# Kernel tuning notes

Hardware: AMD Instinct MI355X
Metric: run time of the kernel (lower is better)

The kernel has to match this reference:

```python
import jax, jax.numpy as jnp
import numpy as np

L, H, C, HS, V, BS = 4, 8, 512, 64, 32000, 2048  # layers, heads, n_embd, head_size, vocab, block_size
B, T = 2, 2048


def _ln(x, g, b, eps=1e-5):
    m = jnp.mean(x, axis=-1, keepdims=True)
    v = jnp.var(x, axis=-1, keepdims=True)
    return (x - m) * jax.lax.rsqrt(v + eps) * g + b


def setup_inputs() -> dict:
    key = jax.random.key(0)
    ks = jax.random.split(key, 12)
    s = 0.02
    f = jnp.float32
    return {
        "idx": jax.random.randint(ks[0], (B, T), 0, V),
        "tok_emb": jax.random.normal(ks[1], (V, C), f) * s,
        "pos_emb": jax.random.normal(ks[2], (BS, C), f) * s,
        "ln1_g": jnp.ones((L, C), f), "ln1_b": jnp.zeros((L, C), f),
        "wq": jax.random.normal(ks[3], (L, H, C, HS), f) * s,
        "wk": jax.random.normal(ks[4], (L, H, C, HS), f) * s,
        "wv": jax.random.normal(ks[5], (L, H, C, HS), f) * s,
        "proj_w": jax.random.normal(ks[6], (L, C, C), f) * s,
        "proj_b": jnp.zeros((L, C), f),
        "ln2_g": jnp.ones((L, C), f), "ln2_b": jnp.zeros((L, C), f),
        "ff_w1": jax.random.normal(ks[7], (L, C, 4 * C), f) * s,
        "ff_b1": jnp.zeros((L, 4 * C), f),
        "ff_w2": jax.random.normal(ks[8], (L, 4 * C, C), f) * s,
        "ff_b2": jnp.zeros((L, C), f),
        "ffln_g": jnp.ones((L, C), f), "ffln_b": jnp.zeros((L, C), f),
        "lm_w": jax.random.normal(ks[9], (C, V), f) * s,
        "lm_b": jnp.zeros((V,), f),
    }


def reference(idx, tok_emb, pos_emb, ln1_g, ln1_b, wq, wk, wv, proj_w, proj_b,
              ln2_g, ln2_b, ff_w1, ff_b1, ff_w2, ff_b2, ffln_g, ffln_b, lm_w, lm_b):
    Tn = idx.shape[1]
    x = tok_emb[idx] + pos_emb[:Tn]  # [B,T,C]
    causal = jnp.tril(jnp.ones((Tn, Tn), bool))
    for l in range(L):
        h = _ln(x, ln1_g[l], ln1_b[l])
        q = jnp.einsum('btc,hcd->bhtd', h, wq[l])
        k = jnp.einsum('btc,hcd->bhtd', h, wk[l])
        v = jnp.einsum('btc,hcd->bhtd', h, wv[l])
        # NOTE: original module does NOT scale by 1/sqrt(head_size)
        wei = jnp.einsum('bhtd,bhsd->bhts', q, k)
        wei = jnp.where(causal, wei, -jnp.inf)
        wei = jax.nn.softmax(wei, axis=-1)
        att = jnp.einsum('bhts,bhsd->bhtd', wei, v)  # [B,H,T,HS]
        att = att.transpose(0, 2, 1, 3).reshape(x.shape[0], Tn, C)
        x = x + att @ proj_w[l].T + proj_b[l]
        h2 = _ln(x, ln2_g[l], ln2_b[l])
        ff = jax.nn.relu(h2 @ ff_w1[l] + ff_b1[l]) @ ff_w2[l] + ff_b2[l]
        ff = _ln(ff, ffln_g[l], ffln_b[l])  # FeedForward has trailing LayerNorm
        x = x + ff
    logits = x @ lm_w + lm_b  # [B,T,V]
    return logits
```

## Files before the change

### kernel.cpp

```cpp
#include <hip/hip_runtime.h>
#include <math.h>

#define NLAYER 4
#define NH     8
#define CDIM   512
#define HS     64
#define VOCAB  32000
#define BB     2
#define TT     2048
#define MROWS  (BB*TT)
#define QKVW   (3*CDIM)

typedef __attribute__((ext_vector_type(8))) short bf16x8;
typedef __attribute__((ext_vector_type(4))) float f32x4;

__device__ __forceinline__ unsigned short f2bf(float f) {
    unsigned int u = __float_as_uint(f);
    u += 0x7FFF + ((u >> 16) & 1);
    return (unsigned short)(u >> 16);
}

#define GLOAD16(g, l) __builtin_amdgcn_global_load_lds( \
    (const __attribute__((address_space(1))) void*)(g), \
    (__attribute__((address_space(3))) void*)(l), 16, 0, 0)

template<int FLAGS, bool OUTBF>
__global__ __launch_bounds__(256) void mfma_gemm(
    const unsigned short* __restrict__ A, int lda,
    const unsigned short* __restrict__ Bt, int ldb,
    const float* __restrict__ bias,
    void* __restrict__ Cout, int ldc,
    const float* __restrict__ resid,
    int K)
{
    __shared__ unsigned short As[128*64];
    __shared__ unsigned short Bs[128*64];
    const int tid = threadIdx.x;
    const int w = tid >> 6, l = tid & 63;
    const int wr = w >> 1, wc = w & 1;
    const long m0 = (long)blockIdx.y * 128;
    const long n0 = (long)blockIdx.x * 128;
    const int srow = l >> 3;
    const int scol = (l & 7) << 3;
    const unsigned short* Ab = A + m0*lda;
    const unsigned short* Bb = Bt + n0*ldb;
    const int fr = l & 15;
    const int fk = (l >> 4) << 3;

    f32x4 acc[4][4];
    #pragma unroll
    for (int m = 0; m < 4; m++)
        #pragma unroll
        for (int n = 0; n < 4; n++) acc[m][n] = (f32x4)0.0f;

    for (int k0 = 0; k0 < K; k0 += 64) {
        __syncthreads();
        #pragma unroll
        for (int i = 0; i < 4; i++) {
            int seg = w*4 + i;
            GLOAD16(Ab + (long)(seg*8 + srow)*lda + k0 + scol, As + seg*512);
            GLOAD16(Bb + (long)(seg*8 + srow)*ldb + k0 + scol, Bs + seg*512);
        }
        __syncthreads();
        #pragma unroll
        for (int kk = 0; kk < 2; kk++) {
            bf16x8 af[4], bf[4];
            #pragma unroll
            for (int m = 0; m < 4; m++)
                af[m] = *(const bf16x8*)&As[(wr*64 + m*16 + fr)*64 + kk*32 + fk];
            #pragma unroll
            for (int n = 0; n < 4; n++)
                bf[n] = *(const bf16x8*)&Bs[(wc*64 + n*16 + fr)*64 + kk*32 + fk];
            #pragma unroll
            for (int m = 0; m < 4; m++)
                #pragma unroll
                for (int n = 0; n < 4; n++)
                    acc[m][n] = __builtin_amdgcn_mfma_f32_16x16x32_bf16(
                        af[m], bf[n], acc[m][n], 0, 0, 0);
        }
    }

    const int rg = (l >> 4) << 2;
    #pragma unroll
    for (int n = 0; n < 4; n++) {
        long gn = n0 + wc*64 + n*16 + fr;
        float bv = (FLAGS & 1) ? bias[gn] : 0.f;
        #pragma unroll
        for (int m = 0; m < 4; m++) {
            #pragma unroll
            for (int r = 0; r < 4; r++) {
                long gm = m0 + wr*64 + m*16 + rg + r;
                float val = acc[m][n][r] + bv;
                if (FLAGS & 2) val = fmaxf(val, 0.f);
                if (FLAGS & 4) val += resid[gm*ldc + gn];
                if (OUTBF) ((unsigned short*)Cout)[gm*ldc + gn] = f2bf(val);
                else       ((float*)Cout)[gm*ldc + gn] = val;
            }
        }
    }
}

__global__ __launch_bounds__(256) void mfma_gemm_qkv(
    const unsigned short* __restrict__ A,
    const unsigned short* __restrict__ Bt,
    unsigned short* __restrict__ qh,
    unsigned short* __restrict__ kh,
    unsigned short* __restrict__ vt)
{
    __shared__ unsigned short As[128*64];
    __shared__ unsigned short Bs[128*64];
    const int tid = threadIdx.x;
    const int w = tid >> 6, l = tid & 63;
    const int wr = w >> 1, wc = w & 1;
    const long m0 = (long)blockIdx.y * 128;
    const long n0 = (long)blockIdx.x * 128;
    const int srow = l >> 3;
    const int scol = (l & 7) << 3;
    const unsigned short* Ab = A + m0*CDIM;
    const unsigned short* Bb = Bt + n0*CDIM;
    const int fr = l & 15;
    const int fk = (l >> 4) << 3;

    f32x4 acc[4][4];
    #pragma unroll
    for (int m = 0; m < 4; m++)
        #pragma unroll
        for (int n = 0; n < 4; n++) acc[m][n] = (f32x4)0.0f;

    for (int k0 = 0; k0 < CDIM; k0 += 64) {
        __syncthreads();
        #pragma unroll
        for (int i = 0; i < 4; i++) {
            int seg = w*4 + i;
            GLOAD16(Ab + (long)(seg*8 + srow)*CDIM + k0 + scol, As + seg*512);
            GLOAD16(Bb + (long)(seg*8 + srow)*CDIM + k0 + scol, Bs + seg*512);
        }
        __syncthreads();
        #pragma unroll
        for (int kk = 0; kk < 2; kk++) {
            bf16x8 af[4], bf[4];
            #pragma unroll
            for (int m = 0; m < 4; m++)
                af[m] = *(const bf16x8*)&As[(wr*64 + m*16 + fr)*64 + kk*32 + fk];
            #pragma unroll
            for (int n = 0; n < 4; n++)
                bf[n] = *(const bf16x8*)&Bs[(wc*64 + n*16 + fr)*64 + kk*32 + fk];
            #pragma unroll
            for (int m = 0; m < 4; m++)
                #pragma unroll
                for (int n = 0; n < 4; n++)
                    acc[m][n] = __builtin_amdgcn_mfma_f32_16x16x32_bf16(
                        af[m], bf[n], acc[m][n], 0, 0, 0);
        }
    }

    const int rg = (l >> 4) << 2;
    #pragma unroll
    for (int n = 0; n < 4; n++) {
        int gn = (int)(n0 + wc*64 + n*16 + fr);
        int which = gn >> 9, hh = (gn >> 6) & 7, d = gn & 63;
        #pragma unroll
        for (int m = 0; m < 4; m++) {
            #pragma unroll
            for (int r = 0; r < 4; r++) {
                int gm = (int)(m0 + wr*64 + m*16 + rg + r);
                int b = gm >> 11, t = gm & (TT-1);
                int head = b*NH + hh;
                unsigned short val = f2bf(acc[m][n][r]);
                if (which == 0)      qh[((long)head*TT + t)*HS + d] = val;
                else if (which == 1) kh[((long)head*TT + t)*HS + d] = val;
                else                 vt[((long)head*HS + d)*TT + t] = val;
            }
        }
    }
}

__global__ __launch_bounds__(256) void attn_mfma(
    const unsigned short* __restrict__ qh,
    const unsigned short* __restrict__ kh,
    const unsigned short* __restrict__ vt,
    unsigned short* __restrict__ att)
{
    __shared__ unsigned short Ks[2][64*64];
    __shared__ unsigned short Vts[2][64*64];
    __shared__ unsigned short Ps[4][32*72];
    const int tid = threadIdx.x;
    const int w = tid >> 6, l = tid & 63;
    const int fr = l & 15, g = l >> 4;
    const int head = blockIdx.y;
    const int b = head >> 3, hh = head & 7;
    const int qt0 = blockIdx.x * 128;
    const int qw = qt0 + w*32;
    const unsigned short* Qb = qh + (long)head*TT*HS;
    const unsigned short* Kb = kh + (long)head*TT*HS;
    const unsigned short* Vb = vt + (long)head*HS*TT;

    bf16x8 aq[2][2];
    #pragma unroll
    for (int mt = 0; mt < 2; mt++)
        #pragma unroll
        for (int ks = 0; ks < 2; ks++)
            aq[mt][ks] = *(const bf16x8*)&Qb[(long)(qw + mt*16 + fr)*HS + ks*32 + g*8];

    f32x4 acc_o[2][4];
    float mrun[2][4], lsum[2][4];
    #pragma unroll
    for (int mt = 0; mt < 2; mt++) {
        #pragma unroll
        for (int r = 0; r < 4; r++) { mrun[mt][r] = -INFINITY; lsum[mt][r] = 0.f; }
        #pragma unroll
        for (int n = 0; n < 4; n++) acc_o[mt][n] = (f32x4)0.0f;
    }

    const int nch = 2*blockIdx.x + 2;
    const int srow = l >> 3;
    const int scol = ((l & 7) ^ (srow & 7)) << 3;

    auto stage = [&](int c, int buf) {
        int s0_ = c*64;
        #pragma unroll
        for (int i = 0; i < 2; i++) {
            int rb = i*32 + w*8;
            GLOAD16(Kb + (long)(s0_ + rb + srow)*HS + scol, &Ks[buf][rb*64]);
            GLOAD16(Vb + (long)(rb + srow)*TT + s0_ + scol, &Vts[buf][rb*64]);
        }
    };

    stage(0, 0);
    for (int c = 0; c < nch; c++) {
        const int s0 = c*64;
        const int buf = c & 1;
        __syncthreads();
        if (c + 1 < nch) stage(c+1, (c+1)&1);
        if (s0 > qw + 31) continue;

        bf16x8 bk[4][2];
        #pragma unroll
        for (int n = 0; n < 4; n++)
            #pragma unroll
            for (int ks = 0; ks < 2; ks++) {
                int row = n*16 + fr;
                int u = (ks*4 + g) ^ (row & 7);
                bk[n][ks] = *(const bf16x8*)&Ks[buf][row*64 + u*8];
            }
        f32x4 sc[2][4];
        #pragma unroll
        for (int mt = 0; mt < 2; mt++)
            #pragma unroll
            for (int n = 0; n < 4; n++) sc[mt][n] = (f32x4)0.0f;
        #pragma unroll
        for (int ks = 0; ks < 2; ks++)
            #pragma unroll
            for (int mt = 0; mt < 2; mt++)
                #pragma unroll
                for (int n = 0; n < 4; n++)
                    sc[mt][n] = __builtin_amdgcn_mfma_f32_16x16x32_bf16(
                        aq[mt][ks], bk[n][ks], sc[mt][n], 0, 0, 0);

        #pragma unroll
        for (int mt = 0; mt < 2; mt++) {
            #pragma unroll
            for (int r = 0; r < 4; r++) {
                int q = qw + mt*16 + g*4 + r;
                float rmax = -INFINITY;
                #pragma unroll
                for (int n = 0; n < 4; n++) {
                    float v = sc[mt][n][r];
                    v = (s0 + n*16 + fr <= q) ? v : -INFINITY;
                    sc[mt][n][r] = v;
                    rmax = fmaxf(rmax, v);
                }
                #pragma unroll
                for (int off = 8; off >= 1; off >>= 1)
                    rmax = fmaxf(rmax, __shfl_xor(rmax, off));
                float mnew = fmaxf(mrun[mt][r], rmax);
                float scale = __expf(mrun[mt][r] - mnew);
                float ps = 0.f;
                #pragma unroll
                for (int n = 0; n < 4; n++) {
                    float p = __expf(sc[mt][n][r] - mnew);
                    sc[mt][n][r] = p;
                    ps += p;
                }
                #pragma unroll
                for (int off = 8; off >= 1; off >>= 1)
                    ps += __shfl_xor(ps, off);
                lsum[mt][r] = lsum[mt][r]*scale + ps;
                mrun[mt][r] = mnew;
                #pragma unroll
                for (int n = 0; n < 4; n++) acc_o[mt][n][r] *= scale;
            }
        }

        #pragma unroll
        for (int mt = 0; mt < 2; mt++)
            #pragma unroll
            for (int n = 0; n < 4; n++)
                #pragma unroll
                for (int r = 0; r < 4; r++)
                    Ps[w][(mt*16 + g*4 + r)*72 + n*16 + fr] = f2bf(sc[mt][n][r]);

        bf16x8 ap[2][2], bv[4][2];
        #pragma unroll
        for (int mt = 0; mt < 2; mt++)
            #pragma unroll
            for (int ks = 0; ks < 2; ks++)
                ap[mt][ks] = *(const bf16x8*)&Ps[w][(mt*16 + fr)*72 + ks*32 + g*8];
        #pragma unroll
        for (int n = 0; n < 4; n++)
            #pragma unroll
            for (int ks = 0; ks < 2; ks++) {
                int row = n*16 + fr;
                int u = (ks*4 + g) ^ (row & 7);
                bv[n][ks] = *(const bf16x8*)&Vts[buf][row*64 + u*8];
            }
        #pragma unroll
        for (int ks = 0; ks < 2; ks++)
            #pragma unroll
            for (int mt = 0; mt < 2; mt++)
                #pragma unroll
                for (int n = 0; n < 4; n++)
                    acc_o[mt][n] = __builtin_amdgcn_mfma_f32_16x16x32_bf16(
                        ap[mt][ks], bv[n][ks], acc_o[mt][n], 0, 0, 0);
    }

    #pragma unroll
    for (int mt = 0; mt < 2; mt++)
        #pragma unroll
        for (int n = 0; n < 4; n++)
            #pragma unroll
            for (int r = 0; r < 4; r++) {
                int t = qw + mt*16 + g*4 + r;
                int d = n*16 + fr;
                att[((long)b*TT + t)*CDIM + hh*HS + d] =
                    f2bf(acc_o[mt][n][r] / lsum[mt][r]);
            }
}

__global__ __launch_bounds__(256) void transpose_cast(
    const float* __restrict__ in, unsigned short* __restrict__ out,
    int R, int Cn, long in_z1, long in_z2, long out_z1, long out_z2, int z2n)
{
    const int z = blockIdx.z;
    const int z1 = z / z2n, z2 = z % z2n;
    const float* ip = in + (long)z1*in_z1 + (long)z2*in_z2;
    unsigned short* op = out + (long)z1*out_z1 + (long)z2*out_z2;
    __shared__ float tile[32][33];
    const int tx = threadIdx.x & 31, ty = threadIdx.x >> 5;
    const long r0 = (long)blockIdx.y*32, c0 = (long)blockIdx.x*32;
    #pragma unroll
    for (int i = 0; i < 4; i++)
        tile[ty + i*8][tx] = ip[(r0 + ty + i*8)*Cn + c0 + tx];
    __syncthreads();
    #pragma unroll
    for (int i = 0; i < 4; i++)
        op[(c0 + ty + i*8)*R + r0 + tx] = f2bf(tile[tx][ty + i*8]);
}

__global__ __launch_bounds__(256) void cast_kernel(
    const float* __restrict__ in, unsigned short* __restrict__ out, long n)
{
    long i = ((long)blockIdx.x*256 + threadIdx.x) * 4;
    if (i >= n) return;
    float4 v = *(const float4*)(in + i);
    ushort4 u = make_ushort4(f2bf(v.x), f2bf(v.y), f2bf(v.z), f2bf(v.w));
    *(ushort4*)(out + i) = u;
}

__global__ void embed_kernel(const int* __restrict__ idx,
                             const float* __restrict__ tok,
                             const float* __restrict__ pos,
                             float* __restrict__ x)
{
    const int r = blockIdx.x;
    const int t = r & (TT-1);
    const long tr = idx[r];
    const float* te = tok + tr*CDIM;
    const float* pe = pos + (long)t*CDIM;
    float* xo = x + (long)r*CDIM;
    for (int c = threadIdx.x; c < CDIM; c += blockDim.x)
        xo[c] = te[c] + pe[c];
}

template<int MODE>
__global__ __launch_bounds__(256) void ln_kernel(
    const float* __restrict__ in, const float* __restrict__ g,
    const float* __restrict__ bb, void* __restrict__ outp)
{
    const int wave = threadIdx.x >> 6;
    const int lane = threadIdx.x & 63;
    const long r = (long)blockIdx.x*4 + wave;
    const float* xr = in + r*CDIM;
    float vals[8];
    float s = 0.f;
    #pragma unroll
    for (int i = 0; i < 8; i++) { vals[i] = xr[lane + i*64]; s += vals[i]; }
    #pragma unroll
    for (int o = 32; o >= 1; o >>= 1) s += __shfl_xor(s, o);
    const float mean = s * (1.f/CDIM);
    float vs = 0.f;
    #pragma unroll
    for (int i = 0; i < 8; i++) { float d = vals[i]-mean; vs += d*d; }
    #pragma unroll
    for (int o = 32; o >= 1; o >>= 1) vs += __shfl_xor(vs, o);
    const float rstd = rsqrtf(vs*(1.f/CDIM) + 1e-5f);
    #pragma unroll
    for (int i = 0; i < 8; i++) {
        int c = lane + i*64;
        float nv = (vals[i]-mean)*rstd*g[c] + bb[c];
        if (MODE == 1) ((unsigned short*)outp)[r*CDIM + c] = f2bf(nv);
        else           ((float*)outp)[r*CDIM + c] += nv;
    }
}

extern "C" void kernel_launch(void* const* d_in, const int* in_sizes, int n_in,
                              void* d_out, int out_size, void* d_ws, size_t ws_size,
                              hipStream_t stream)
{
    const int*   idx   = (const int*)  d_in[0];
    const float* tok   = (const float*)d_in[1];
    const float* pos   = (const float*)d_in[2];
    const float* ln1g  = (const float*)d_in[3];
    const float* ln1b  = (const float*)d_in[4];
    const float* wq    = (const float*)d_in[5];
    const float* wk    = (const float*)d_in[6];
    const float* wv    = (const float*)d_in[7];
    const float* projw = (const float*)d_in[8];
    const float* projb = (const float*)d_in[9];
    const float* ln2g  = (const float*)d_in[10];
    const float* ln2b  = (const float*)d_in[11];
    const float* ffw1  = (const float*)d_in[12];
    const float* ffb1  = (const float*)d_in[13];
    const float* ffw2  = (const float*)d_in[14];
    const float* ffb2  = (const float*)d_in[15];
    const float* flng  = (const float*)d_in[16];
    const float* flnb  = (const float*)d_in[17];
    const float* lmw   = (const float*)d_in[18];
    const float* lmb   = (const float*)d_in[19];
    float* out = (float*)d_out;

    char* wp = (char*)d_ws;
    float* x  = (float*)wp;           wp += (size_t)MROWS*CDIM*4;
    float* ff = (float*)wp;           wp += (size_t)MROWS*CDIM*4;
    unsigned short* h     = (unsigned short*)wp; wp += (size_t)MROWS*CDIM*2;
    unsigned short* lmt   = (unsigned short*)wp; wp += (size_t)VOCAB*CDIM*2;
    unsigned short* ff1t  = (unsigned short*)wp; wp += (size_t)NLAYER*4*CDIM*CDIM*2;
    unsigned short* ff2t  = (unsigned short*)wp; wp += (size_t)NLAYER*4*CDIM*CDIM*2;
    unsigned short* qkvt  = (unsigned short*)wp; wp += (size_t)NLAYER*QKVW*CDIM*2;
    unsigned short* projc = (unsigned short*)wp; wp += (size_t)NLAYER*CDIM*CDIM*2;
    unsigned short* qh    = (unsigned short*)wp; wp += (size_t)BB*NH*TT*HS*2;
    unsigned short* kh    = (unsigned short*)wp; wp += (size_t)BB*NH*TT*HS*2;
    unsigned short* vt    = (unsigned short*)wp; wp += (size_t)BB*NH*TT*HS*2;

    unsigned short* f1  = (unsigned short*)d_out;
    unsigned short* att = f1 + (size_t)MROWS*4*CDIM;

    transpose_cast<<<dim3(VOCAB/32, CDIM/32, 1), 256, 0, stream>>>(
        lmw, lmt, CDIM, VOCAB, 0, 0, 0, 0, 1);
    transpose_cast<<<dim3(4*CDIM/32, CDIM/32, NLAYER), 256, 0, stream>>>(
        ffw1, ff1t, CDIM, 4*CDIM, (long)CDIM*4*CDIM, 0, (long)4*CDIM*CDIM, 0, 1);
    transpose_cast<<<dim3(CDIM/32, 4*CDIM/32, NLAYER), 256, 0, stream>>>(
        ffw2, ff2t, 4*CDIM, CDIM, (long)4*CDIM*CDIM, 0, (long)CDIM*4*CDIM, 0, 1);
    {
        const size_t QBLK = (size_t)CDIM * CDIM;
        transpose_cast<<<dim3(HS/32, CDIM/32, NLAYER*NH), 256, 0, stream>>>(
            wq, qkvt,            CDIM, HS,
            (long)NH*CDIM*HS, (long)CDIM*HS, (long)QKVW*CDIM, (long)HS*CDIM, NH);
        transpose_cast<<<dim3(HS/32, CDIM/32, NLAYER*NH), 256, 0, stream>>>(
            wk, qkvt + QBLK,     CDIM, HS,
            (long)NH*CDIM*HS, (long)CDIM*HS, (long)QKVW*CDIM, (long)HS*CDIM, NH);
        transpose_cast<<<dim3(HS/32, CDIM/32, NLAYER*NH), 256, 0, stream>>>(
            wv, qkvt + 2*QBLK,   CDIM, HS,
            (long)NH*CDIM*HS, (long)CDIM*HS, (long)QKVW*CDIM, (long)HS*CDIM, NH);
    }
    cast_kernel<<<(NLAYER*CDIM*CDIM/4 + 255)/256, 256, 0, stream>>>(
        projw, projc, (long)NLAYER*CDIM*CDIM);

    embed_kernel<<<MROWS, 256, 0, stream>>>(idx, tok, pos, x);

    for (int l = 0; l < NLAYER; l++) {
        const unsigned short* qkvt_l = qkvt + (size_t)l*QKVW*CDIM;
        const unsigned short* projc_l = projc + (size_t)l*CDIM*CDIM;
        const unsigned short* ff1t_l = ff1t + (size_t)l*4*CDIM*CDIM;
        const unsigned short* ff2t_l = ff2t + (size_t)l*4*CDIM*CDIM;

        ln_kernel<1><<<MROWS/4, 256, 0, stream>>>(x, ln1g + l*CDIM, ln1b + l*CDIM, h);

        mfma_gemm_qkv<<<dim3(QKVW/128, MROWS/128), 256, 0, stream>>>(
            h, qkvt_l, qh, kh, vt);

        attn_mfma<<<dim3(TT/128, BB*NH), 256, 0, stream>>>(qh, kh, vt, att);

        mfma_gemm<5,false><<<dim3(CDIM/128, MROWS/128), 256, 0, stream>>>(
            att, CDIM, projc_l, CDIM, projb + l*CDIM, x, CDIM, x, CDIM);

        ln_kernel<1><<<MROWS/4, 256, 0, stream>>>(x, ln2g + l*CDIM, ln2b + l*CDIM, h);

        mfma_gemm<3,true><<<dim3(4*CDIM/128, MROWS/128), 256, 0, stream>>>(
            h, CDIM, ff1t_l, CDIM, ffb1 + (size_t)l*4*CDIM, f1, 4*CDIM, nullptr, CDIM);

        mfma_gemm<1,false><<<dim3(CDIM/128, MROWS/128), 256, 0, stream>>>(
            f1, 4*CDIM, ff2t_l, 4*CDIM, ffb2 + l*CDIM, ff, CDIM, nullptr, 4*CDIM);

        ln_kernel<2><<<MROWS/4, 256, 0, stream>>>(ff, flng + l*CDIM, flnb + l*CDIM, x);
    }

    cast_kernel<<<(MROWS*CDIM/4 + 255)/256, 256, 0, stream>>>(x, h, (long)MROWS*CDIM);
    mfma_gemm<1,false><<<dim3(VOCAB/128, MROWS/128), 256, 0, stream>>>(
        h, CDIM, lmt, CDIM, lmb, out, VOCAB, nullptr, CDIM);
}
```

Measured before the change: 1.132 ms.

## Split attention KV range in two and merge partials; fuse final cast into LN

```diff
diff --git a/kernel.cpp b/kernel.cpp
--- a/kernel.cpp
+++ b/kernel.cpp
@@ -10,6 +10,7 @@
 #define TT     2048
 #define MROWS  (BB*TT)
 #define QKVW   (3*CDIM)
+#define NHEADS (BB*NH)
 
 typedef __attribute__((ext_vector_type(8))) short bf16x8;
 typedef __attribute__((ext_vector_type(4))) float f32x4;
@@ -175,11 +176,11 @@
     }
 }
 
-__global__ __launch_bounds__(256) void attn_mfma(
+__global__ __launch_bounds__(256) void attn_part(
     const unsigned short* __restrict__ qh,
     const unsigned short* __restrict__ kh,
     const unsigned short* __restrict__ vt,
-    unsigned short* __restrict__ att)
+    float* __restrict__ oP, float* __restrict__ ml)
 {
     __shared__ unsigned short Ks[2][64*64];
     __shared__ unsigned short Vts[2][64*64];
@@ -188,8 +189,9 @@
     const int w = tid >> 6, l = tid & 63;
     const int fr = l & 15, g = l >> 4;
     const int head = blockIdx.y;
-    const int b = head >> 3, hh = head & 7;
-    const int qt0 = blockIdx.x * 128;
+    const int sp = blockIdx.z;
+    const int x = blockIdx.x;
+    const int qt0 = x * 128;
     const int qw = qt0 + w*32;
     const unsigned short* Qb = qh + (long)head*TT*HS;
     const unsigned short* Kb = kh + (long)head*TT*HS;
@@ -212,11 +214,13 @@
         for (int n = 0; n < 4; n++) acc_o[mt][n] = (f32x4)0.0f;
     }
 
-    const int nch = 2*blockIdx.x + 2;
+    const int cbeg = sp * (x + 1);
+    const int cend = cbeg + (x + 1);
     const int srow = l >> 3;
     const int scol = ((l & 7) ^ (srow & 7)) << 3;
 
-    auto stage = [&](int c, int buf) {
+    auto stage = [&](int c) {
+        int buf = c & 1;
         int s0_ = c*64;
         #pragma unroll
         for (int i = 0; i < 2; i++) {
@@ -226,12 +230,12 @@
         }
     };
 
-    stage(0, 0);
-    for (int c = 0; c < nch; c++) {
+    stage(cbeg);
+    for (int c = cbeg; c < cend; c++) {
         const int s0 = c*64;
         const int buf = c & 1;
         __syncthreads();
-        if (c + 1 < nch) stage(c+1, (c+1)&1);
+        if (c + 1 < cend) stage(c+1);
         if (s0 > qw + 31) continue;
 
         bf16x8 bk[4][2];
@@ -324,17 +328,43 @@
                         ap[mt][ks], bv[n][ks], acc_o[mt][n], 0, 0, 0);
     }
 
-    #pragma unroll
-    for (int mt = 0; mt < 2; mt++)
+    float* oB = oP + ((long)(head*2 + sp)*TT)*HS;
+    float* mlB = ml + ((long)(head*2 + sp)*TT)*2;
+    #pragma unroll
+    for (int mt = 0; mt < 2; mt++) {
         #pragma unroll
         for (int n = 0; n < 4; n++)
+            #pragma unroll
+            for (int r = 0; r < 4; r++)
+                oB[(long)(qw + mt*16 + g*4 + r)*HS + n*16 + fr] = acc_o[mt][n][r];
+        if (fr == 0) {
             #pragma unroll
             for (int r = 0; r < 4; r++) {
                 int t = qw + mt*16 + g*4 + r;
-                int d = n*16 + fr;
-                att[((long)b*TT + t)*CDIM + hh*HS + d] =
-                    f2bf(acc_o[mt][n][r] / lsum[mt][r]);
+                mlB[t*2]     = mrun[mt][r];
+                mlB[t*2 + 1] = lsum[mt][r];
             }
+        }
+    }
+}
+
+__global__ __launch_bounds__(256) void attn_combine(
+    const float* __restrict__ oP, const float* __restrict__ ml,
+    unsigned short* __restrict__ att)
+{
+    const int gid = blockIdx.x*4 + (threadIdx.x >> 6);
+    const int lane = threadIdx.x & 63;
+    const int head = gid >> 11, t = gid & (TT-1);
+    const int b = head >> 3, hh = head & 7;
+    const long i0 = (long)(head*2 + 0)*TT + t;
+    const long i1 = (long)(head*2 + 1)*TT + t;
+    const float m0 = ml[i0*2], l0 = ml[i0*2+1];
+    const float m1 = ml[i1*2], l1 = ml[i1*2+1];
+    const float M = fmaxf(m0, m1);
+    const float e0 = __expf(m0 - M), e1 = __expf(m1 - M);
+    const float L = l0*e0 + l1*e1;
+    const float v = (oP[i0*HS + lane]*e0 + oP[i1*HS + lane]*e1) / L;
+    att[((long)b*TT + t)*CDIM + hh*HS + lane] = f2bf(v);
 }
 
 __global__ __launch_bounds__(256) void transpose_cast(
@@ -385,7 +415,8 @@
 template<int MODE>
 __global__ __launch_bounds__(256) void ln_kernel(
     const float* __restrict__ in, const float* __restrict__ g,
-    const float* __restrict__ bb, void* __restrict__ outp)
+    const float* __restrict__ bb, void* __restrict__ outp,
+    void* __restrict__ outp2)
 {
     const int wave = threadIdx.x >> 6;
     const int lane = threadIdx.x & 63;
@@ -408,8 +439,13 @@
     for (int i = 0; i < 8; i++) {
         int c = lane + i*64;
         float nv = (vals[i]-mean)*rstd*g[c] + bb[c];
-        if (MODE == 1) ((unsigned short*)outp)[r*CDIM + c] = f2bf(nv);
-        else           ((float*)outp)[r*CDIM + c] += nv;
+        if (MODE == 1) {
+            ((unsigned short*)outp)[r*CDIM + c] = f2bf(nv);
+        } else {
+            float s2 = ((float*)outp)[r*CDIM + c] + nv;
+            ((float*)outp)[r*CDIM + c] = s2;
+            if (MODE == 3) ((unsigned short*)outp2)[r*CDIM + c] = f2bf(s2);
+        }
     }
 }
 
@@ -448,12 +484,14 @@
     unsigned short* ff2t  = (unsigned short*)wp; wp += (size_t)NLAYER*4*CDIM*CDIM*2;
     unsigned short* qkvt  = (unsigned short*)wp; wp += (size_t)NLAYER*QKVW*CDIM*2;
     unsigned short* projc = (unsigned short*)wp; wp += (size_t)NLAYER*CDIM*CDIM*2;
-    unsigned short* qh    = (unsigned short*)wp; wp += (size_t)BB*NH*TT*HS*2;
-    unsigned short* kh    = (unsigned short*)wp; wp += (size_t)BB*NH*TT*HS*2;
-    unsigned short* vt    = (unsigned short*)wp; wp += (size_t)BB*NH*TT*HS*2;
+    unsigned short* qh    = (unsigned short*)wp; wp += (size_t)NHEADS*TT*HS*2;
+    unsigned short* kh    = (unsigned short*)wp; wp += (size_t)NHEADS*TT*HS*2;
+    unsigned short* vt    = (unsigned short*)wp; wp += (size_t)NHEADS*TT*HS*2;
 
     unsigned short* f1  = (unsigned short*)d_out;
     unsigned short* att = f1 + (size_t)MROWS*4*CDIM;
+    float* oP = (float*)(att + (size_t)MROWS*CDIM);
+    float* ml = oP + (size_t)NHEADS*2*TT*HS;
 
     transpose_cast<<<dim3(VOCAB/32, CDIM/32, 1), 256, 0, stream>>>(
         lmw, lmt, CDIM, VOCAB, 0, 0, 0, 0, 1);
@@ -484,17 +522,18 @@
         const unsigned short* ff1t_l = ff1t + (size_t)l*4*CDIM*CDIM;
         const unsigned short* ff2t_l = ff2t + (size_t)l*4*CDIM*CDIM;
 
-        ln_kernel<1><<<MROWS/4, 256, 0, stream>>>(x, ln1g + l*CDIM, ln1b + l*CDIM, h);
+        ln_kernel<1><<<MROWS/4, 256, 0, stream>>>(x, ln1g + l*CDIM, ln1b + l*CDIM, h, nullptr);
 
         mfma_gemm_qkv<<<dim3(QKVW/128, MROWS/128), 256, 0, stream>>>(
             h, qkvt_l, qh, kh, vt);
 
-        attn_mfma<<<dim3(TT/128, BB*NH), 256, 0, stream>>>(qh, kh, vt, att);
+        attn_part<<<dim3(TT/128, NHEADS, 2), 256, 0, stream>>>(qh, kh, vt, oP, ml);
+        attn_combine<<<dim3(NHEADS*TT/4), 256, 0, stream>>>(oP, ml, att);
 
         mfma_gemm<5,false><<<dim3(CDIM/128, MROWS/128), 256, 0, stream>>>(
             att, CDIM, projc_l, CDIM, projb + l*CDIM, x, CDIM, x, CDIM);
 
-        ln_kernel<1><<<MROWS/4, 256, 0, stream>>>(x, ln2g + l*CDIM, ln2b + l*CDIM, h);
+        ln_kernel<1><<<MROWS/4, 256, 0, stream>>>(x, ln2g + l*CDIM, ln2b + l*CDIM, h, nullptr);
 
         mfma_gemm<3,true><<<dim3(4*CDIM/128, MROWS/128), 256, 0, stream>>>(
             h, CDIM, ff1t_l, CDIM, ffb1 + (size_t)l*4*CDIM, f1, 4*CDIM, nullptr, CDIM);
@@ -502,10 +541,12 @@
         mfma_gemm<1,false><<<dim3(CDIM/128, MROWS/128), 256, 0, stream>>>(
             f1, 4*CDIM, ff2t_l, 4*CDIM, ffb2 + l*CDIM, ff, CDIM, nullptr, 4*CDIM);
 
-        ln_kernel<2><<<MROWS/4, 256, 0, stream>>>(ff, flng + l*CDIM, flnb + l*CDIM, x);
-    }
-
-    cast_kernel<<<(MROWS*CDIM/4 + 255)/256, 256, 0, stream>>>(x, h, (long)MROWS*CDIM);
+        if (l == NLAYER-1)
+            ln_kernel<3><<<MROWS/4, 256, 0, stream>>>(ff, flng + l*CDIM, flnb + l*CDIM, x, h);
+        else
+            ln_kernel<2><<<MROWS/4, 256, 0, stream>>>(ff, flng + l*CDIM, flnb + l*CDIM, x, nullptr);
+    }
+
     mfma_gemm<1,false><<<dim3(VOCAB/128, MROWS/128), 256, 0, stream>>>(
         h, CDIM, lmt, CDIM, lmb, out, VOCAB, nullptr, CDIM);
 }
```

After: 1.034 ms. -8.7%, faster.
